# Kernel optimization log

Measured on AMD Instinct MI355X. Metric: run time of the kernel, lower is better.

The kernel has to match this reference:

```python
import jax, jax.numpy as jnp
import numpy as np
from jax import lax

BN_EPS = 1e-5
SQ_EPS = 1e-8


def squash(s, axis=-1):
    # v = (|s|^2 / (1+|s|^2)) * s / |s|
    n2 = jnp.sum(s * s, axis=axis, keepdims=True)
    return (n2 / (1.0 + n2)) * s / jnp.sqrt(n2 + SQ_EPS)


def setup_inputs() -> dict:
    key = jax.random.key(0)
    ks = jax.random.split(key, 5)
    B, C, H, W = 64, 512, 28, 28
    NUM_ROUTES = 8 * 10 * 10  # lower_num_caps * 10 * 10 after k9 s2 conv on 28x28
    features = jax.random.normal(ks[0], (B, C, H, W), jnp.float32)
    conv1_w = jax.random.normal(ks[1], (256, 512, 3, 3), jnp.float32) * 0.02
    conv1_b = jnp.zeros((256,), jnp.float32)
    bn_gamma = jnp.ones((256,), jnp.float32)
    bn_beta = jnp.zeros((256,), jnp.float32)
    bn_mean = jnp.zeros((256,), jnp.float32)
    bn_var = jnp.ones((256,), jnp.float32)
    prim_w = jax.random.normal(ks[2], (256, 256, 9, 9), jnp.float32) * 0.02
    prim_b = jnp.zeros((256,), jnp.float32)
    # routing transform: (num_routes, higher_num_caps, out_dim, in_dim)
    route_w = jax.random.normal(ks[3], (NUM_ROUTES, 2, 16, 32), jnp.float32) * 0.05
    return {"features": features, "conv1_w": conv1_w, "conv1_b": conv1_b,
            "bn_gamma": bn_gamma, "bn_beta": bn_beta, "bn_mean": bn_mean,
            "bn_var": bn_var, "prim_w": prim_w, "prim_b": prim_b,
            "route_w": route_w}


def reference(features, conv1_w, conv1_b, bn_gamma, bn_beta, bn_mean, bn_var,
              prim_w, prim_b, route_w):
    B = features.shape[0]
    dn = ("NCHW", "OIHW", "NCHW")
    # pre_conv: Conv2d(512->256, k3, pad1) + BatchNorm (eval) + ReLU
    x = lax.conv_general_dilated(features, conv1_w, (1, 1), "SAME",
                                 dimension_numbers=dn)
    x = x + conv1_b[None, :, None, None]
    inv = bn_gamma * lax.rsqrt(bn_var + BN_EPS)
    x = x * inv[None, :, None, None] + (bn_beta - bn_mean * inv)[None, :, None, None]
    x = jax.nn.relu(x)
    # primary capsules: Conv2d(256->8*32, k9, s2, valid) -> (B,256,10,10)
    p = lax.conv_general_dilated(x, prim_w, (2, 2), "VALID",
                                 dimension_numbers=dn)
    p = p + prim_b[None, :, None, None]
    Hp, Wp = p.shape[2], p.shape[3]
    # (B, num_caps, cap_dim, Hp*Wp) -> (B, num_caps*Hp*Wp, cap_dim)
    p = p.reshape(B, 8, 32, Hp * Wp).transpose(0, 1, 3, 2).reshape(B, 8 * Hp * Wp, 32)
    lower_caps = squash(p, axis=-1)  # (B, 800, 32)
    # predictions u_hat: (B, routes, higher_caps, out_dim)
    u_hat = jnp.einsum("bri,rjoi->brjo", lower_caps, route_w)
    # dynamic routing-by-agreement
    b = jnp.zeros((B, u_hat.shape[1], u_hat.shape[2]), u_hat.dtype)
    n_iter = 3
    for it in range(n_iter):
        c = jax.nn.softmax(b, axis=2)                  # coupling coeffs
        s = jnp.einsum("brj,brjo->bjo", c, u_hat)      # weighted sum
        v = squash(s, axis=-1)                          # (B, 2, 16)
        if it < n_iter - 1:
            b = b + jnp.einsum("brjo,bjo->brj", u_hat, v)
    return (lower_caps, v)
```

## Files before the change

kernel.cpp:

```cpp
#include <hip/hip_runtime.h>
#include <hip/hip_bf16.h>

#define BN_EPS 1e-5f
#define SQ_EPS 1e-8f

typedef __hip_bfloat16 bf16;
typedef __attribute__((ext_vector_type(8))) short bf16x8;
typedef __attribute__((ext_vector_type(4))) float f32x4;

__device__ __forceinline__ void gload_lds16(const void* g, void* l) {
    __builtin_amdgcn_global_load_lds(
        (const __attribute__((address_space(1))) unsigned int*)g,
        (__attribute__((address_space(3))) unsigned int*)l, 16, 0, 0);
}

__device__ __forceinline__ unsigned short f2bfu(float f) {
    bf16 h = __float2bfloat16(f);
    return *(unsigned short*)&h;
}

__global__ __launch_bounds__(256) void feat_to_nhwc(
    const float* __restrict__ feat, bf16* __restrict__ featP) {
    int b = blockIdx.z, ct = blockIdx.y, pt = blockIdx.x;
    int ci0 = ct * 64, px0 = pt * 64;
    int tid = threadIdx.x;
    __shared__ float t[64][65];
#pragma unroll
    for (int rep = 0; rep < 16; rep++) {
        int ci_l = rep * 4 + (tid >> 6);
        int px = px0 + (tid & 63);
        float v = 0.f;
        if (px < 784) v = feat[(b * 512 + ci0 + ci_l) * 784 + px];
        t[ci_l][tid & 63] = v;
    }
    __syncthreads();
#pragma unroll
    for (int rep = 0; rep < 4; rep++) {
        int px_l = rep * 16 + (tid >> 4);
        int px = px0 + px_l;
        if (px < 784) {
            int h = px / 28, wq = px % 28;
            int ci = (tid & 15) * 4;
            ushort4 o;
            o.x = f2bfu(t[ci + 0][px_l]);
            o.y = f2bfu(t[ci + 1][px_l]);
            o.z = f2bfu(t[ci + 2][px_l]);
            o.w = f2bfu(t[ci + 3][px_l]);
            *(ushort4*)&featP[((b * 30 + h + 1) * 30 + (wq + 1)) * 512 + ci0 + ci] = o;
        }
    }
}

__global__ __launch_bounds__(256) void wF_transform(
    const float* __restrict__ w1, const float* __restrict__ w2,
    bf16* __restrict__ wt1F, bf16* __restrict__ wt2F,
    bf16* __restrict__ featP) {
    __shared__ float tt[10368];
    if (blockIdx.x >= 768) {
        int b = blockIdx.x - 768;
        uint4 zz = {0u, 0u, 0u, 0u};
        for (int i = threadIdx.x; i < 116 * 64; i += 256) {
            int rp = i >> 6;
            int ci = (i & 63) * 8;
            int hp, wp;
            if (rp < 30)      { hp = 0;       wp = rp; }
            else if (rp < 60) { hp = 29;      wp = rp - 30; }
            else if (rp < 88) { hp = rp - 59; wp = 0; }
            else              { hp = rp - 87; wp = 29; }
            *(uint4*)&featP[(b * 900 + hp * 30 + wp) * 512 + ci] = zz;
        }
        return;
    }
    if (blockIdx.x < 256) {
        int co = blockIdx.x;
        const float* src = w1 + co * 4608;
        for (int i = threadIdx.x; i < 4608; i += 256) tt[i] = src[i];
        __syncthreads();
        int co16 = co >> 4, l15 = co & 15;
        for (int i = threadIdx.x; i < 576; i += 256) {
            int g = i >> 6, cc = (i >> 2) & 15, kq = i & 3;
            short v[8];
#pragma unroll
            for (int j = 0; j < 8; j++) {
                unsigned short u = f2bfu(tt[(cc * 32 + kq * 8 + j) * 9 + g]);
                v[j] = (short)u;
            }
            int fidx = cc * 9 + g;
            bf16x8* dst = (bf16x8*)&wt1F[(fidx * 16 + co16) * 512 + (kq * 16 + l15) * 8];
            bf16x8 pk = {v[0], v[1], v[2], v[3], v[4], v[5], v[6], v[7]};
            *dst = pk;
        }
    } else {
        int bid = blockIdx.x - 256;
        int half = bid & 1, co = bid >> 1;
        const float* src = w2 + co * 20736 + half * 10368;
        for (int i = threadIdx.x; i < 10368; i += 256) tt[i] = src[i];
        __syncthreads();
        int co16 = co >> 4, l15 = co & 15;
        for (int i = threadIdx.x; i < 1296; i += 256) {
            int sh = i >> 4, ccl = (i >> 2) & 3, kq = i & 3;
            int z = sh / 10; if (z > 7) z = 7;
            int s0 = (81 * z) >> 3;
            int ns = ((81 * (z + 1)) >> 3) - s0;
            int fidx = s0 * 8 + (half * 4 + ccl) * ns + (sh - s0);
            short v[8];
#pragma unroll
            for (int j = 0; j < 8; j++) {
                unsigned short u = f2bfu(tt[(ccl * 32 + kq * 8 + j) * 81 + sh]);
                v[j] = (short)u;
            }
            bf16x8* dst = (bf16x8*)&wt2F[(fidx * 16 + co16) * 512 + (kq * 16 + l15) * 8];
            bf16x8 pk = {v[0], v[1], v[2], v[3], v[4], v[5], v[6], v[7]};
            *dst = pk;
        }
    }
}

__global__ __launch_bounds__(512, 4) void conv1_mfma(
    const bf16* __restrict__ featP, const bf16* __restrict__ wt1F,
    const float* __restrict__ bias, const float* __restrict__ gamma,
    const float* __restrict__ beta, const float* __restrict__ mean,
    const float* __restrict__ var, bf16* __restrict__ x) {
    __shared__ char As4[4 * 7168];
    const int tid = threadIdx.x, lane = tid & 63, w = tid >> 6;
    const int Mt = blockIdx.x;

    const bf16* pA0;
    {
        int r0 = (w << 4) + (lane >> 2);
        int q = (lane & 3) ^ ((r0 >> 1) & 3);
        int m0 = Mt * 112 + (w < 7 ? r0 : 0);
        int b0 = m0 / 784, rr = m0 % 784, h0 = rr / 28, w0 = rr % 28;
        pA0 = featP + ((b0 * 30 + h0) * 30 + w0) * 512 + q * 8;
    }
    const bf16x8* pB = (const bf16x8*)wt1F + w * 128 + lane;

    int a_off[7];
#pragma unroll
    for (int mi = 0; mi < 7; mi++) {
        int r = mi * 16 + (lane & 15);
        a_off[mi] = r * 64 + (((lane >> 4) ^ ((r >> 1) & 3)) * 16);
    }

    f32x4 acc[7][2];
#pragma unroll
    for (int i = 0; i < 7; i++)
#pragma unroll
        for (int j = 0; j < 2; j++) acc[i][j] = f32x4{0.f, 0.f, 0.f, 0.f};

    bf16x8 Bv0[2], Bv1[2];

#define STG1(bi, offE)                                                     \
    do {                                                                   \
        if (w < 7)                                                         \
            gload_lds16(pA0 + (offE), As4 + (bi) * 7168 + w * 1024);       \
    } while (0)

    STG1(0, 0); STG1(1, 512); STG1(2, 1024);
    { const bf16x8* bp = pB; Bv0[0] = bp[0]; Bv0[1] = bp[64]; }
    asm volatile("s_waitcnt vmcnt(2)" ::: "memory");
    __builtin_amdgcn_s_barrier();
    asm volatile("" ::: "memory");

#define C1_STEP(u, BU, BL)                                                 \
    do {                                                                   \
        const int t_ = t + (u);                                            \
        int ttc = t_ + 3; if (ttc > 143) ttc = 143;                        \
        {                                                                  \
            int cc_ = ttc / 9, g_ = ttc - 9 * cc_;                         \
            int ky_ = g_ / 3, kx_ = g_ - 3 * ky_;                          \
            STG1((u + 3) & 3, (ky_ * 30 + kx_) * 512 + cc_ * 32);          \
        }                                                                  \
        {                                                                  \
            int fn = t_ + 1; if (fn > 143) fn = 143;                       \
            const bf16x8* bp = pB + fn * 1024;                             \
            BL[0] = bp[0]; BL[1] = bp[64];                                 \
        }                                                                  \
        const char* Ab = As4 + (u) * 7168;                                 \
        bf16x8 af[7];                                                      \
        _Pragma("unroll")                                                  \
        for (int mi = 0; mi < 7; mi++)                                     \
            af[mi] = *(const bf16x8*)(Ab + a_off[mi]);                     \
        _Pragma("unroll")                                                  \
        for (int nj = 0; nj < 2; nj++)                                     \
            _Pragma("unroll")                                              \
            for (int mi = 0; mi < 7; mi++)                                 \
                acc[mi][nj] = __builtin_amdgcn_mfma_f32_16x16x32_bf16(     \
                    af[mi], BU[nj], acc[mi][nj], 0, 0, 0);                 \
        if (t_ < 143) {                                                    \
            asm volatile("s_waitcnt vmcnt(8)" ::: "memory");               \
            __builtin_amdgcn_s_barrier();                                  \
            asm volatile("" ::: "memory");                                 \
        }                                                                  \
    } while (0)

    for (int t = 0; t < 144; t += 4) {
        C1_STEP(0, Bv0, Bv1);
        C1_STEP(1, Bv1, Bv0);
        C1_STEP(2, Bv0, Bv1);
        C1_STEP(3, Bv1, Bv0);
    }

#pragma unroll
    for (int nj = 0; nj < 2; nj++) {
        int co = w * 32 + nj * 16 + (lane & 15);
        float inv = gamma[co] * rsqrtf(var[co] + BN_EPS);
        float sh = beta[co] - mean[co] * inv;
        float bs = bias[co];
#pragma unroll
        for (int mi = 0; mi < 7; mi++) {
            int m0 = Mt * 112 + mi * 16 + ((lane >> 4) << 2);
#pragma unroll
            for (int r = 0; r < 4; r++) {
                float v = (acc[mi][nj][r] + bs) * inv + sh;
                x[(m0 + r) * 256 + co] = __float2bfloat16(fmaxf(v, 0.f));
            }
        }
    }
#undef STG1
#undef C1_STEP
}

__global__ __launch_bounds__(512, 4) void conv2_mfma(
    const bf16* __restrict__ x, const bf16* __restrict__ wt2F,
    bf16* __restrict__ p_parts) {
    __shared__ char As4[4 * 7168];
    const int tid = threadIdx.x, lane = tid & 63, w = tid >> 6;
    const int z = blockIdx.x & 7, Mt = blockIdx.x >> 3;
    const int sh0 = (81 * z) >> 3, sh1 = (81 * (z + 1)) >> 3;
    const int nsh = sh1 - sh0;
    const int NT = nsh << 3;
    const int FB = sh0 << 3;

    const bf16* pA0;
    {
        int r0 = (w << 4) + (lane >> 2);
        int rr = (w < 7) ? r0 : 0;
        int s = rr < 100 ? rr : 99;
        int q = (lane & 3) ^ ((rr >> 1) & 3);
        int ho = s / 10, wo = s - ho * 10;
        pA0 = x + ((Mt * 28 + 2 * ho) * 28 + 2 * wo) * 256 + q * 8;
    }
    const bf16x8* pB = (const bf16x8*)wt2F + w * 128 + lane;

    int a_off[7];
#pragma unroll
    for (int mi = 0; mi < 7; mi++) {
        int r = mi * 16 + (lane & 15);
        a_off[mi] = r * 64 + (((lane >> 4) ^ ((r >> 1) & 3)) * 16);
    }

    f32x4 acc[7][2];
#pragma unroll
    for (int i = 0; i < 7; i++)
#pragma unroll
        for (int j = 0; j < 2; j++) acc[i][j] = f32x4{0.f, 0.f, 0.f, 0.f};

    bf16x8 Bv0[2], Bv1[2];

#define STG2(bi, offE)                                                     \
    do {                                                                   \
        if (w < 7)                                                         \
            gload_lds16(pA0 + (offE), As4 + (bi) * 7168 + w * 1024);       \
    } while (0)

#define A2OFF(tt)                                                          \
    ({ int ttc_ = (tt) < NT ? (tt) : NT - 1;                               \
       int cc_ = ttc_ / nsh, si_ = ttc_ - cc_ * nsh;                       \
       int sh_ = sh0 + si_;                                                \
       int ky_ = sh_ / 9, kx_ = sh_ - 9 * ky_;                             \
       (ky_ * 28 + kx_) * 256 + cc_ * 32; })

    STG2(0, A2OFF(0)); STG2(1, A2OFF(1)); STG2(2, A2OFF(2));
    { const bf16x8* bp = pB + FB * 1024; Bv0[0] = bp[0]; Bv0[1] = bp[64]; }
    asm volatile("s_waitcnt vmcnt(2)" ::: "memory");
    __builtin_amdgcn_s_barrier();
    asm volatile("" ::: "memory");

#define C2_STEP(u, BU, BL)                                                 \
    do {                                                                   \
        const int t_ = t + (u);                                            \
        STG2((u + 3) & 3, A2OFF(t_ + 3));                                  \
        {                                                                  \
            int fn = t_ + 1; if (fn > NT - 1) fn = NT - 1;                 \
            const bf16x8* bp = pB + (FB + fn) * 1024;                      \
            BL[0] = bp[0]; BL[1] = bp[64];                                 \
        }                                                                  \
        const char* Ab = As4 + (u) * 7168;                                 \
        bf16x8 af[7];                                                      \
        _Pragma("unroll")                                                  \
        for (int mi = 0; mi < 7; mi++)                                     \
            af[mi] = *(const bf16x8*)(Ab + a_off[mi]);                     \
        _Pragma("unroll")                                                  \
        for (int nj = 0; nj < 2; nj++)                                     \
            _Pragma("unroll")                                              \
            for (int mi = 0; mi < 7; mi++)                                 \
                acc[mi][nj] = __builtin_amdgcn_mfma_f32_16x16x32_bf16(     \
                    af[mi], BU[nj], acc[mi][nj], 0, 0, 0);                 \
        if (t_ < NT - 1) {                                                 \
            asm volatile("s_waitcnt vmcnt(8)" ::: "memory");               \
            __builtin_amdgcn_s_barrier();                                  \
            asm volatile("" ::: "memory");                                 \
        }                                                                  \
    } while (0)

    for (int t = 0; t < NT; t += 4) {
        C2_STEP(0, Bv0, Bv1);
        C2_STEP(1, Bv1, Bv0);
        C2_STEP(2, Bv0, Bv1);
        C2_STEP(3, Bv1, Bv0);
    }

#pragma unroll
    for (int nj = 0; nj < 2; nj++) {
        int co = w * 32 + nj * 16 + (lane & 15);
#pragma unroll
        for (int mi = 0; mi < 7; mi++) {
            int row0 = mi * 16 + ((lane >> 4) << 2);
#pragma unroll
            for (int r = 0; r < 4; r++) {
                int row = row0 + r;
                if (row < 100)
                    p_parts[(z * 6400 + Mt * 100 + row) * 256 + co] =
                        __float2bfloat16(acc[mi][nj][r]);
            }
        }
    }
#undef STG2
#undef A2OFF
#undef C2_STEP
}

__global__ __launch_bounds__(256) void squash_uhat(
    const bf16* __restrict__ pp, const float* __restrict__ pb,
    const float* __restrict__ rw, float* __restrict__ lc,
    bf16* __restrict__ uht) {
    int rT = blockIdx.x, bT = blockIdx.y;
    int rl = threadIdx.x >> 5, jo = threadIdx.x & 31;
    int r = rT * 8 + rl;
    float4 wreg[8];
    const float4* wp4 = (const float4*)(rw + (r * 32 + jo) * 32);
#pragma unroll
    for (int k = 0; k < 8; k++) wreg[k] = wp4[k];
    int cap = r / 100, s = r - cap * 100;
    int co = cap * 32 + jo;
    float bsv = pb[co];
    __shared__ float vrow[8][32];
    for (int b = bT * 16; b < bT * 16 + 16; b++) {
        int m = b * 100 + s;
        float val = bsv;
#pragma unroll
        for (int zz = 0; zz < 8; zz++)
            val += __bfloat162float(pp[(zz * 6400 + m) * 256 + co]);
        float n2 = val * val;
#pragma unroll
        for (int msk = 1; msk < 32; msk <<= 1) n2 += __shfl_xor(n2, msk);
        float scale = n2 / ((1.f + n2) * sqrtf(n2 + SQ_EPS));
        float sval = val * scale;
        lc[(b * 800 + r) * 32 + jo] = sval;
        vrow[rl][jo] = sval;
        float acc = 0.f;
#pragma unroll
        for (int k = 0; k < 8; k++) {
            float4 a = *(const float4*)&vrow[rl][k * 4];
            acc = fmaf(a.x, wreg[k].x, acc);
            acc = fmaf(a.y, wreg[k].y, acc);
            acc = fmaf(a.z, wreg[k].z, acc);
            acc = fmaf(a.w, wreg[k].w, acc);
        }
        uht[(b * 32 + jo) * 800 + r] = __float2bfloat16(acc);
    }
}

__global__ __launch_bounds__(256) void route_all(
    const bf16* __restrict__ uht, float* __restrict__ vout) {
    extern __shared__ float rs[];
    float* u = rs;
    float* lg = rs + 26400;
    float* red = lg + 1600;
    float* vs = red + 256;
    int b = blockIdx.x, tid = threadIdx.x;
    for (int i = tid; i < 25600; i += 256) {
        int jo = i / 800, r = i - jo * 800;
        u[r * 33 + jo] = __bfloat162float(uht[(b * 32 + jo) * 800 + r]);
    }
    for (int i = tid; i < 1600; i += 256) lg[i] = 0.f;
    __syncthreads();
    int jo = tid & 31, rg = tid >> 5;
    for (int it = 0; it < 3; it++) {
        float sp = 0.f;
        for (int r = rg; r < 800; r += 8) {
            float l0 = lg[r * 2], l1 = lg[r * 2 + 1];
            float m = fmaxf(l0, l1);
            float e0 = __expf(l0 - m), e1 = __expf(l1 - m);
            float c = ((jo < 16) ? e0 : e1) / (e0 + e1);
            sp += c * u[r * 33 + jo];
        }
        red[rg * 32 + jo] = sp;
        __syncthreads();
        if (tid < 32) {
            float s = 0.f;
#pragma unroll
            for (int k = 0; k < 8; k++) s += red[k * 32 + tid];
            float n2 = s * s;
#pragma unroll
            for (int m = 1; m < 16; m <<= 1) n2 += __shfl_xor(n2, m);
            float scale = n2 / ((1.f + n2) * sqrtf(n2 + SQ_EPS));
            float v = s * scale;
            vs[tid] = v;
            if (it == 2) vout[b * 32 + tid] = v;
        }
        __syncthreads();
        if (it < 2) {
            for (int r = tid; r < 800; r += 256) {
                float d0 = 0.f, d1 = 0.f;
#pragma unroll
                for (int o = 0; o < 16; o++) {
                    d0 += u[r * 33 + o] * vs[o];
                    d1 += u[r * 33 + 16 + o] * vs[16 + o];
                }
                lg[r * 2] += d0;
                lg[r * 2 + 1] += d1;
            }
            __syncthreads();
        }
    }
}

extern "C" void kernel_launch(void* const* d_in, const int* in_sizes, int n_in,
                              void* d_out, int out_size, void* d_ws, size_t ws_size,
                              hipStream_t stream) {
    const float* feat    = (const float*)d_in[0];
    const float* conv1_w = (const float*)d_in[1];
    const float* conv1_b = (const float*)d_in[2];
    const float* bn_g    = (const float*)d_in[3];
    const float* bn_b    = (const float*)d_in[4];
    const float* bn_m    = (const float*)d_in[5];
    const float* bn_v    = (const float*)d_in[6];
    const float* prim_w  = (const float*)d_in[7];
    const float* prim_b  = (const float*)d_in[8];
    const float* route_w = (const float*)d_in[9];
    float* out = (float*)d_out;

    char* wsb = (char*)d_ws;
    bf16*  featP   = (bf16*)(wsb + 0);
    bf16*  p_parts = (bf16*)(wsb + 0);
    bf16*  uht     = (bf16*)(wsb + 26214400);
    bf16*  x       = (bf16*)(wsb + 58982400);
    bf16*  wt1F    = (bf16*)(wsb + 84672512);
    bf16*  wt2F    = (bf16*)(wsb + 87031808);

    float* lc_out = out;
    float* v_out  = out + 64 * 800 * 32;

    hipFuncSetAttribute((const void*)route_all,
                        hipFuncAttributeMaxDynamicSharedMemorySize, 113152);

    feat_to_nhwc<<<dim3(13, 8, 64), 256, 0, stream>>>(feat, featP);
    wF_transform<<<832, 256, 0, stream>>>(conv1_w, prim_w, wt1F, wt2F, featP);

    conv1_mfma<<<448, 512, 0, stream>>>(
        featP, wt1F, conv1_b, bn_g, bn_b, bn_m, bn_v, x);

    conv2_mfma<<<512, 512, 0, stream>>>(x, wt2F, p_parts);

    squash_uhat<<<dim3(100, 4), 256, 0, stream>>>(
        p_parts, prim_b, route_w, lc_out, uht);

    route_all<<<64, 256, 113152, stream>>>(uht, v_out);
}
```

Baseline: 286.9 us.

## Merge prep kernels into one launch and widen squash/routing parallelism

Merges the feature NHWC transpose, the weight re-layout and the border zeroing into a single prep_all launch, with block ranges dispatched by blockIdx. This removes one kernel launch and the serialisation gap between the two prep kernels. It also doubles squash_uhat's grid by giving each block 8 batches instead of 16. route_all moves to 512 threads with a larger reduction buffer. The merged kernel now declares both shared arrays, so its static LDS footprint and occupancy may change.

```diff
diff --git a/kernel.cpp b/kernel.cpp
--- a/kernel.cpp
+++ b/kernel.cpp
@@ -19,47 +19,46 @@
     return *(unsigned short*)&h;
 }
 
-__global__ __launch_bounds__(256) void feat_to_nhwc(
-    const float* __restrict__ feat, bf16* __restrict__ featP) {
-    int b = blockIdx.z, ct = blockIdx.y, pt = blockIdx.x;
-    int ci0 = ct * 64, px0 = pt * 64;
+__global__ __launch_bounds__(256) void prep_all(
+    const float* __restrict__ feat, const float* __restrict__ w1,
+    const float* __restrict__ w2, bf16* __restrict__ featP,
+    bf16* __restrict__ wt1F, bf16* __restrict__ wt2F) {
     int tid = threadIdx.x;
-    __shared__ float t[64][65];
-#pragma unroll
-    for (int rep = 0; rep < 16; rep++) {
-        int ci_l = rep * 4 + (tid >> 6);
-        int px = px0 + (tid & 63);
-        float v = 0.f;
-        if (px < 784) v = feat[(b * 512 + ci0 + ci_l) * 784 + px];
-        t[ci_l][tid & 63] = v;
-    }
-    __syncthreads();
-#pragma unroll
-    for (int rep = 0; rep < 4; rep++) {
-        int px_l = rep * 16 + (tid >> 4);
-        int px = px0 + px_l;
-        if (px < 784) {
-            int h = px / 28, wq = px % 28;
-            int ci = (tid & 15) * 4;
-            ushort4 o;
-            o.x = f2bfu(t[ci + 0][px_l]);
-            o.y = f2bfu(t[ci + 1][px_l]);
-            o.z = f2bfu(t[ci + 2][px_l]);
-            o.w = f2bfu(t[ci + 3][px_l]);
-            *(ushort4*)&featP[((b * 30 + h + 1) * 30 + (wq + 1)) * 512 + ci0 + ci] = o;
-        }
-    }
-}
-
-__global__ __launch_bounds__(256) void wF_transform(
-    const float* __restrict__ w1, const float* __restrict__ w2,
-    bf16* __restrict__ wt1F, bf16* __restrict__ wt2F,
-    bf16* __restrict__ featP) {
-    __shared__ float tt[10368];
-    if (blockIdx.x >= 768) {
-        int b = blockIdx.x - 768;
+    if (blockIdx.x < 6656) {
+        int bid = blockIdx.x;
+        int pt = bid % 13, ct = (bid / 13) & 7, b = bid / 104;
+        int ci0 = ct * 64, px0 = pt * 64;
+        __shared__ float t[64][65];
+#pragma unroll
+        for (int rep = 0; rep < 16; rep++) {
+            int ci_l = rep * 4 + (tid >> 6);
+            int px = px0 + (tid & 63);
+            float v = 0.f;
+            if (px < 784) v = feat[(b * 512 + ci0 + ci_l) * 784 + px];
+            t[ci_l][tid & 63] = v;
+        }
+        __syncthreads();
+#pragma unroll
+        for (int rep = 0; rep < 4; rep++) {
+            int px_l = rep * 16 + (tid >> 4);
+            int px = px0 + px_l;
+            if (px < 784) {
+                int h = px / 28, wq = px % 28;
+                int ci = (tid & 15) * 4;
+                ushort4 o;
+                o.x = f2bfu(t[ci + 0][px_l]);
+                o.y = f2bfu(t[ci + 1][px_l]);
+                o.z = f2bfu(t[ci + 2][px_l]);
+                o.w = f2bfu(t[ci + 3][px_l]);
+                *(ushort4*)&featP[((b * 30 + h + 1) * 30 + (wq + 1)) * 512 + ci0 + ci] = o;
+            }
+        }
+        return;
+    }
+    if (blockIdx.x >= 7424) {
+        int b = blockIdx.x - 7424;
         uint4 zz = {0u, 0u, 0u, 0u};
-        for (int i = threadIdx.x; i < 116 * 64; i += 256) {
+        for (int i = tid; i < 116 * 64; i += 256) {
             int rp = i >> 6;
             int ci = (i & 63) * 8;
             int hp, wp;
@@ -71,13 +70,14 @@
         }
         return;
     }
-    if (blockIdx.x < 256) {
-        int co = blockIdx.x;
+    __shared__ float tt[10368];
+    if (blockIdx.x < 6912) {
+        int co = blockIdx.x - 6656;
         const float* src = w1 + co * 4608;
-        for (int i = threadIdx.x; i < 4608; i += 256) tt[i] = src[i];
+        for (int i = tid; i < 4608; i += 256) tt[i] = src[i];
         __syncthreads();
         int co16 = co >> 4, l15 = co & 15;
-        for (int i = threadIdx.x; i < 576; i += 256) {
+        for (int i = tid; i < 576; i += 256) {
             int g = i >> 6, cc = (i >> 2) & 15, kq = i & 3;
             short v[8];
 #pragma unroll
@@ -91,13 +91,13 @@
             *dst = pk;
         }
     } else {
-        int bid = blockIdx.x - 256;
+        int bid = blockIdx.x - 6912;
         int half = bid & 1, co = bid >> 1;
         const float* src = w2 + co * 20736 + half * 10368;
-        for (int i = threadIdx.x; i < 10368; i += 256) tt[i] = src[i];
+        for (int i = tid; i < 10368; i += 256) tt[i] = src[i];
         __syncthreads();
         int co16 = co >> 4, l15 = co & 15;
-        for (int i = threadIdx.x; i < 1296; i += 256) {
+        for (int i = tid; i < 1296; i += 256) {
             int sh = i >> 4, ccl = (i >> 2) & 3, kq = i & 3;
             int z = sh / 10; if (z > 7) z = 7;
             int s0 = (81 * z) >> 3;
@@ -346,7 +346,7 @@
     int co = cap * 32 + jo;
     float bsv = pb[co];
     __shared__ float vrow[8][32];
-    for (int b = bT * 16; b < bT * 16 + 16; b++) {
+    for (int b = bT * 8; b < bT * 8 + 8; b++) {
         int m = b * 100 + s;
         float val = bsv;
 #pragma unroll
@@ -372,24 +372,24 @@
     }
 }
 
-__global__ __launch_bounds__(256) void route_all(
+__global__ __launch_bounds__(512) void route_all(
     const bf16* __restrict__ uht, float* __restrict__ vout) {
     extern __shared__ float rs[];
     float* u = rs;
     float* lg = rs + 26400;
     float* red = lg + 1600;
-    float* vs = red + 256;
+    float* vs = red + 512;
     int b = blockIdx.x, tid = threadIdx.x;
-    for (int i = tid; i < 25600; i += 256) {
+    for (int i = tid; i < 25600; i += 512) {
         int jo = i / 800, r = i - jo * 800;
         u[r * 33 + jo] = __bfloat162float(uht[(b * 32 + jo) * 800 + r]);
     }
-    for (int i = tid; i < 1600; i += 256) lg[i] = 0.f;
+    for (int i = tid; i < 1600; i += 512) lg[i] = 0.f;
     __syncthreads();
     int jo = tid & 31, rg = tid >> 5;
     for (int it = 0; it < 3; it++) {
         float sp = 0.f;
-        for (int r = rg; r < 800; r += 8) {
+        for (int r = rg; r < 800; r += 16) {
             float l0 = lg[r * 2], l1 = lg[r * 2 + 1];
             float m = fmaxf(l0, l1);
             float e0 = __expf(l0 - m), e1 = __expf(l1 - m);
@@ -401,7 +401,7 @@
         if (tid < 32) {
             float s = 0.f;
 #pragma unroll
-            for (int k = 0; k < 8; k++) s += red[k * 32 + tid];
+            for (int k = 0; k < 16; k++) s += red[k * 32 + tid];
             float n2 = s * s;
 #pragma unroll
             for (int m = 1; m < 16; m <<= 1) n2 += __shfl_xor(n2, m);
@@ -412,7 +412,7 @@
         }
         __syncthreads();
         if (it < 2) {
-            for (int r = tid; r < 800; r += 256) {
+            for (int r = tid; r < 800; r += 512) {
                 float d0 = 0.f, d1 = 0.f;
 #pragma unroll
                 for (int o = 0; o < 16; o++) {
@@ -454,18 +454,17 @@
     float* v_out  = out + 64 * 800 * 32;
 
     hipFuncSetAttribute((const void*)route_all,
-                        hipFuncAttributeMaxDynamicSharedMemorySize, 113152);
-
-    feat_to_nhwc<<<dim3(13, 8, 64), 256, 0, stream>>>(feat, featP);
-    wF_transform<<<832, 256, 0, stream>>>(conv1_w, prim_w, wt1F, wt2F, featP);
+                        hipFuncAttributeMaxDynamicSharedMemorySize, 114304);
+
+    prep_all<<<7488, 256, 0, stream>>>(feat, conv1_w, prim_w, featP, wt1F, wt2F);
 
     conv1_mfma<<<448, 512, 0, stream>>>(
         featP, wt1F, conv1_b, bn_g, bn_b, bn_m, bn_v, x);
 
     conv2_mfma<<<512, 512, 0, stream>>>(x, wt2F, p_parts);
 
-    squash_uhat<<<dim3(100, 4), 256, 0, stream>>>(
+    squash_uhat<<<dim3(100, 8), 256, 0, stream>>>(
         p_parts, prim_b, route_w, lc_out, uht);
 
-    route_all<<<64, 256, 113152, stream>>>(uht, v_out);
-}
+    route_all<<<64, 512, 114304, stream>>>(uht, v_out);
+}
```

Result: slower. 307.5 us (+7.2%).
